# Kernel tuning notes

Measured on AMD Instinct MI355X. Metric: run time of the kernel, lower is better.

Reference implementation:

```python
import jax, jax.numpy as jnp
import numpy as np

S = 3072      # total tokens across all images
DIM = 1280    # hidden_size
H = 16        # num_heads
HD = DIM // H # head_dim = 80
NSEG = 6      # number of images (cu_seqlens has NSEG+1 entries)


def _rotate_half(x):
    x1, x2 = jnp.split(x, 2, axis=-1)
    return jnp.concatenate([-x2, x1], axis=-1)


def setup_inputs() -> dict:
    key = jax.random.key(0)
    ks = jax.random.split(key, 12)
    hidden_states = jax.random.normal(ks[0], (S, DIM), jnp.float32)
    # realistic vision rotary embedding: half-dim inv_freq, repeated to head_dim
    inv_freq = 1.0 / (10000.0 ** (jnp.arange(0, HD // 2, dtype=jnp.float32) / (HD // 2)))
    freqs = jnp.arange(S, dtype=jnp.float32)[:, None] * inv_freq[None, :]  # [S, HD/2]
    emb = jnp.concatenate([freqs, freqs], axis=-1)  # [S, HD]
    cos = jnp.cos(emb)
    sin = jnp.sin(emb)
    sc = 0.02
    wq = jax.random.normal(ks[1], (DIM, DIM), jnp.float32) * sc
    bq = jax.random.normal(ks[2], (DIM,), jnp.float32) * sc
    wk = jax.random.normal(ks[3], (DIM, DIM), jnp.float32) * sc
    bk = jax.random.normal(ks[4], (DIM,), jnp.float32) * sc
    wv = jax.random.normal(ks[5], (DIM, DIM), jnp.float32) * sc
    bv = jax.random.normal(ks[6], (DIM,), jnp.float32) * sc
    wo = jax.random.normal(ks[7], (DIM, DIM), jnp.float32) * sc
    bo = jax.random.normal(ks[8], (DIM,), jnp.float32) * sc
    cu_seqlens = (jnp.arange(NSEG + 1, dtype=jnp.int32) * (S // NSEG))  # [0,512,...,3072]
    return dict(hidden_states=hidden_states, cos=cos, sin=sin,
                wq=wq, bq=bq, wk=wk, bk=bk, wv=wv, bv=bv, wo=wo, bo=bo,
                cu_seqlens=cu_seqlens)


def reference(hidden_states, cos, sin, wq, bq, wk, bk, wv, bv, wo, bo, cu_seqlens):
    seq_length = hidden_states.shape[0]
    scaling = HD ** (-0.5)
    # QKV projections (torch Linear: x @ W.T + b)
    q = (hidden_states @ wq.T + bq).reshape(seq_length, H, HD)
    k = (hidden_states @ wk.T + bk).reshape(seq_length, H, HD)
    v = (hidden_states @ wv.T + bv).reshape(seq_length, H, HD)
    # apply_rotary_pos_emb_vision: cos/sin [S, HD] broadcast over head axis
    c = cos[:, None, :]
    s = sin[:, None, :]
    q = q * c + _rotate_half(q) * s
    k = k * c + _rotate_half(k) * s
    # block-diagonal (per-image) attention via segment mask
    seg = jnp.searchsorted(cu_seqlens[1:], jnp.arange(seq_length), side='right')
    mask = seg[:, None] == seg[None, :]  # [S, S] bool
    scores = jnp.einsum('shd,thd->hst', q, k) * scaling  # [H, S, S]
    scores = jnp.where(mask[None, :, :], scores, jnp.finfo(scores.dtype).min)
    attn = jax.nn.softmax(scores, axis=-1)
    out = jnp.einsum('hst,thd->shd', attn, v).reshape(seq_length, DIM)
    return out @ wo.T + bo
```

## Files before the change

kernel.cpp:

```cpp
#include <hip/hip_runtime.h>
#include <hip/hip_bf16.h>
#include <hip/hip_fp16.h>
#include <cstdint>
#include <cstddef>

typedef _Float16 f16;
typedef f16 f16x4 __attribute__((ext_vector_type(4)));
typedef f16 f16x8 __attribute__((ext_vector_type(8)));
typedef float f32x4 __attribute__((ext_vector_type(4)));

#define S_LEN 3072
#define DIM 1280
#define NH 16
#define HD 80
#define SEG 512

#define MFMA16F(a, b, c) __builtin_amdgcn_mfma_f32_16x16x32_f16((a), (b), (c), 0, 0, 0)

__device__ __forceinline__ void gl2lds16(const void* g, void* l) {
    __builtin_amdgcn_global_load_lds(
        (const __attribute__((address_space(1))) unsigned int*)g,
        (__attribute__((address_space(3))) unsigned int*)l, 16, 0, 0);
}

__global__ __launch_bounds__(256) void cvt_kernel(
    const float* __restrict__ hs,
    const float* __restrict__ wq, const float* __restrict__ wk,
    const float* __restrict__ wv, const float* __restrict__ wo,
    f16* __restrict__ hs16,
    f16* __restrict__ wq16, f16* __restrict__ wk16,
    f16* __restrict__ wv16, f16* __restrict__ wo16)
{
    const int m = blockIdx.y;
    const float* src; f16* dst; int n4;
    if (m == 0)      { src = hs; dst = hs16; n4 = S_LEN * DIM / 4; }
    else if (m == 1) { src = wq; dst = wq16; n4 = DIM * DIM / 4; }
    else if (m == 2) { src = wk; dst = wk16; n4 = DIM * DIM / 4; }
    else if (m == 3) { src = wv; dst = wv16; n4 = DIM * DIM / 4; }
    else             { src = wo; dst = wo16; n4 = DIM * DIM / 4; }
    int idx = blockIdx.x * 256 + threadIdx.x;
    if (idx >= n4) return;
    f32x4 v = *(const f32x4*)(src + (size_t)idx * 4);
    f16x4 o;
#pragma unroll
    for (int e = 0; e < 4; ++e) o[e] = (f16)v[e];
    *(f16x4*)(dst + (size_t)idx * 4) = o;
}

__global__ __launch_bounds__(256) void gemm_f16_kernel(
    const f16* __restrict__ A,
    const f16* __restrict__ W0, const f16* __restrict__ W1, const f16* __restrict__ W2,
    const float* __restrict__ b0, const float* __restrict__ b1, const float* __restrict__ b2,
    f16* __restrict__ O0, f16* __restrict__ O1, f16* __restrict__ O2,
    float* __restrict__ OF, int mode_base)
{
    const int mode = mode_base + blockIdx.z;
    const f16* W = (mode == 1) ? W1 : (mode == 2) ? W2 : W0;
    const float* bias = (mode == 1) ? b1 : (mode == 2) ? b2 : b0;

    __shared__ __align__(16) f16 As[128 * 32];
    __shared__ __align__(16) f16 Bs[128 * 32];

    const int tid = threadIdx.x;
    const int lane = tid & 63;
    const int lane15 = tid & 15;
    const int quad = lane >> 4;
    const int w = tid >> 6;
    const int wm = (w >> 1) * 64;
    const int wn = (w & 1) * 64;
    const int m0 = blockIdx.x * 128;
    const int n0 = blockIdx.y * 128;

    const int srow = w * 32 + (lane >> 2);
    const int scol = (lane & 3) * 8;
    const f16* gA0 = A + (size_t)(m0 + srow) * DIM + scol;
    const f16* gA1 = A + (size_t)(m0 + srow + 16) * DIM + scol;
    const f16* gB0 = W + (size_t)(n0 + srow) * DIM + scol;
    const f16* gB1 = W + (size_t)(n0 + srow + 16) * DIM + scol;
    f16* lA0 = As + (w * 32) * 32;
    f16* lA1 = As + (w * 32 + 16) * 32;
    f16* lB0 = Bs + (w * 32) * 32;
    f16* lB1 = Bs + (w * 32 + 16) * 32;

    f32x4 acc[4][4];
#pragma unroll
    for (int i = 0; i < 4; ++i)
#pragma unroll
        for (int j = 0; j < 4; ++j)
            acc[i][j] = (f32x4){0.f, 0.f, 0.f, 0.f};

    for (int kt = 0; kt < DIM / 32; ++kt) {
        __syncthreads();
        gl2lds16(gA0 + kt * 32, lA0);
        gl2lds16(gA1 + kt * 32, lA1);
        gl2lds16(gB0 + kt * 32, lB0);
        gl2lds16(gB1 + kt * 32, lB1);
        __syncthreads();

        f16x8 fa[4], fb[4];
#pragma unroll
        for (int i = 0; i < 4; ++i)
            fa[i] = *(const f16x8*)(As + (wm + i * 16 + lane15) * 32 + quad * 8);
#pragma unroll
        for (int j = 0; j < 4; ++j)
            fb[j] = *(const f16x8*)(Bs + (wn + j * 16 + lane15) * 32 + quad * 8);
#pragma unroll
        for (int i = 0; i < 4; ++i)
#pragma unroll
            for (int j = 0; j < 4; ++j)
                acc[i][j] = MFMA16F(fa[i], fb[j], acc[i][j]);
    }

    float bvv[4];
#pragma unroll
    for (int j = 0; j < 4; ++j)
        bvv[j] = bias[n0 + wn + j * 16 + lane15];

    if (mode == 3) {
#pragma unroll
        for (int i = 0; i < 4; ++i)
#pragma unroll
            for (int j = 0; j < 4; ++j)
#pragma unroll
                for (int r = 0; r < 4; ++r) {
                    int row = m0 + wm + i * 16 + quad * 4 + r;
                    int col = n0 + wn + j * 16 + lane15;
                    OF[(size_t)row * DIM + col] = acc[i][j][r] + bvv[j];
                }
    } else {
        f16* O = (mode == 0) ? O0 : (mode == 1) ? O1 : O2;
#pragma unroll
        for (int i = 0; i < 4; ++i)
#pragma unroll
            for (int j = 0; j < 4; ++j)
#pragma unroll
                for (int r = 0; r < 4; ++r) {
                    int row = m0 + wm + i * 16 + quad * 4 + r;
                    int col = n0 + wn + j * 16 + lane15;
                    O[(size_t)row * DIM + col] = (f16)(acc[i][j][r] + bvv[j]);
                }
    }
}

__global__ __launch_bounds__(256) void vtrans_kernel(
    const f16* __restrict__ v, f16* __restrict__ vT)
{
    const int h = blockIdx.x;
    const int s0 = blockIdx.y * 128;
    __shared__ __align__(16) f16 Ls[128 * 128];
    const int tid = threadIdx.x;
#pragma unroll
    for (int c = tid; c < 1280; c += 256) {
        int r = c / 10;
        int ch = c - r * 10;
        int chs = ch ^ ((r >> 3) & 7);
        *(f16x8*)(Ls + r * 128 + chs * 8) =
            *(const f16x8*)(v + (size_t)(s0 + r) * DIM + h * HD + ch * 8);
    }
    __syncthreads();
#pragma unroll
    for (int c = tid; c < 1280; c += 256) {
        int d = c >> 4;
        int sc = c & 15;
        f16x8 ov;
#pragma unroll
        for (int e = 0; e < 8; ++e) {
            int s = sc * 8 + e;
            ov[e] = Ls[s * 128 + (((d >> 3) ^ (sc & 7)) * 8) + (d & 7)];
        }
        *(f16x8*)(vT + (size_t)(h * HD + d) * S_LEN + s0 + sc * 8) = ov;
    }
}

__global__ __launch_bounds__(256) void rope_kernel(
    f16* __restrict__ qb, f16* __restrict__ kb,
    const float* __restrict__ cosb, const float* __restrict__ sinb)
{
    int idx = blockIdx.x * 256 + threadIdx.x;
    int c = idx % 5;
    int t = idx / 5;
    int h = t & 15; t >>= 4;
    int s = t % S_LEN;
    int which = t / S_LEN;
    f16* buf = which ? kb : qb;
    float scale = which ? 1.0f : 0.11180339887498948f;
    int j = c * 8;
    f32x4 ca = *(const f32x4*)(cosb + s * HD + j);
    f32x4 cb = *(const f32x4*)(cosb + s * HD + j + 4);
    f32x4 sna = *(const f32x4*)(sinb + s * HD + j);
    f32x4 snb = *(const f32x4*)(sinb + s * HD + j + 4);
    size_t base = (size_t)s * DIM + h * HD + j;
    f16x8 x1 = *(f16x8*)(buf + base);
    f16x8 x2 = *(f16x8*)(buf + base + 40);
    f16x8 o1, o2;
#pragma unroll
    for (int e = 0; e < 8; ++e) {
        float ce = (e < 4) ? ca[e] : cb[e - 4];
        float se = (e < 4) ? sna[e] : snb[e - 4];
        float a = (float)x1[e], b = (float)x2[e];
        o1[e] = (f16)((a * ce - b * se) * scale);
        o2[e] = (f16)((b * ce + a * se) * scale);
    }
    *(f16x8*)(buf + base) = o1;
    *(f16x8*)(buf + base + 40) = o2;
}

__global__ __launch_bounds__(256) void attn_kernel(
    const f16* __restrict__ q, const f16* __restrict__ k,
    const f16* __restrict__ vT, f16* __restrict__ o)
{
    const int h = blockIdx.x;
    const int g = blockIdx.y;
    const int qc = blockIdx.z;
    const int tid = threadIdx.x;
    const int lane15 = tid & 15;
    const int quad = (tid & 63) >> 4;
    const int w = tid >> 6;
    const int qbase = g * SEG + qc * 128;

    __shared__ __align__(16) f16 Ks[128 * 88];
    __shared__ __align__(16) f16 Vt[80 * 136];
    __shared__ __align__(16) f16 Ps[4][16 * 136];

    f16x8 zf;
#pragma unroll
    for (int e = 0; e < 8; ++e) zf[e] = (f16)0.0f;

    f16x8 fq[2][3];
#pragma unroll
    for (int mt = 0; mt < 2; ++mt) {
        const int row = qbase + w * 32 + mt * 16 + lane15;
#pragma unroll
        for (int kc = 0; kc < 3; ++kc) {
            if (kc == 2 && quad >= 2) fq[mt][kc] = zf;
            else fq[mt][kc] = *(const f16x8*)(q + (size_t)row * DIM + h * HD + kc * 32 + quad * 8);
        }
    }

    float m_run[2][4], l_run[2][4];
    f32x4 Oa[2][5];
#pragma unroll
    for (int mt = 0; mt < 2; ++mt) {
#pragma unroll
        for (int r = 0; r < 4; ++r) { m_run[mt][r] = -1e30f; l_run[mt][r] = 0.f; }
#pragma unroll
        for (int nt = 0; nt < 5; ++nt) Oa[mt][nt] = (f32x4){0.f, 0.f, 0.f, 0.f};
    }

    for (int kt = 0; kt < 4; ++kt) {
        __syncthreads();
        const int kb = g * SEG + kt * 128;
#pragma unroll
        for (int c = tid; c < 1280; c += 256) {
            int r = c / 10;
            int c8 = (c - r * 10) * 8;
            *(f16x8*)(Ks + r * 88 + c8) =
                *(const f16x8*)(k + (size_t)(kb + r) * DIM + h * HD + c8);
        }
#pragma unroll
        for (int c = tid; c < 1280; c += 256) {
            int d = c >> 4;
            int sc = (c & 15) * 8;
            *(f16x8*)(Vt + d * 136 + sc) =
                *(const f16x8*)(vT + (size_t)(h * HD + d) * S_LEN + kb + sc);
        }
        __syncthreads();

        f32x4 sa[2][8];
#pragma unroll
        for (int mt = 0; mt < 2; ++mt)
#pragma unroll
            for (int nt = 0; nt < 8; ++nt) sa[mt][nt] = (f32x4){0.f, 0.f, 0.f, 0.f};
#pragma unroll
        for (int kc = 0; kc < 3; ++kc) {
#pragma unroll
            for (int nt = 0; nt < 8; ++nt) {
                f16x8 fk;
                if (kc == 2 && quad >= 2) fk = zf;
                else fk = *(const f16x8*)(Ks + (nt * 16 + lane15) * 88 + kc * 32 + quad * 8);
                sa[0][nt] = MFMA16F(fq[0][kc], fk, sa[0][nt]);
                sa[1][nt] = MFMA16F(fq[1][kc], fk, sa[1][nt]);
            }
        }

#pragma unroll
        for (int mt = 0; mt < 2; ++mt) {
            float mtv[4];
#pragma unroll
            for (int r = 0; r < 4; ++r) mtv[r] = -1e30f;
#pragma unroll
            for (int nt = 0; nt < 8; ++nt)
#pragma unroll
                for (int r = 0; r < 4; ++r) mtv[r] = fmaxf(mtv[r], sa[mt][nt][r]);
#pragma unroll
            for (int off = 1; off < 16; off <<= 1)
#pragma unroll
                for (int r = 0; r < 4; ++r)
                    mtv[r] = fmaxf(mtv[r], __shfl_xor(mtv[r], off, 64));

            float alpha[4], lt[4];
#pragma unroll
            for (int r = 0; r < 4; ++r) {
                float mn = fmaxf(m_run[mt][r], mtv[r]);
                alpha[r] = __expf(m_run[mt][r] - mn);
                m_run[mt][r] = mn;
                lt[r] = 0.f;
            }
#pragma unroll
            for (int nt = 0; nt < 8; ++nt)
#pragma unroll
                for (int r = 0; r < 4; ++r) {
                    float p = __expf(sa[mt][nt][r] - m_run[mt][r]);
                    sa[mt][nt][r] = p;
                    lt[r] += p;
                }
#pragma unroll
            for (int off = 1; off < 16; off <<= 1)
#pragma unroll
                for (int r = 0; r < 4; ++r)
                    lt[r] += __shfl_xor(lt[r], off, 64);
#pragma unroll
            for (int r = 0; r < 4; ++r)
                l_run[mt][r] = l_run[mt][r] * alpha[r] + lt[r];

#pragma unroll
            for (int nt = 0; nt < 8; ++nt)
#pragma unroll
                for (int r = 0; r < 4; ++r)
                    Ps[w][(quad * 4 + r) * 136 + nt * 16 + lane15] = (f16)sa[mt][nt][r];

#pragma unroll
            for (int nt = 0; nt < 5; ++nt)
#pragma unroll
                for (int r = 0; r < 4; ++r) Oa[mt][nt][r] *= alpha[r];
#pragma unroll
            for (int kc2 = 0; kc2 < 4; ++kc2) {
                f16x8 fp = *(const f16x8*)(Ps[w] + lane15 * 136 + kc2 * 32 + quad * 8);
#pragma unroll
                for (int nt = 0; nt < 5; ++nt) {
                    f16x8 fv = *(const f16x8*)(Vt + (nt * 16 + lane15) * 136 + kc2 * 32 + quad * 8);
                    Oa[mt][nt] = MFMA16F(fp, fv, Oa[mt][nt]);
                }
            }
        }
    }

#pragma unroll
    for (int mt = 0; mt < 2; ++mt)
#pragma unroll
        for (int r = 0; r < 4; ++r) {
            float inv = 1.0f / l_run[mt][r];
            int row = qbase + w * 32 + mt * 16 + quad * 4 + r;
#pragma unroll
            for (int nt = 0; nt < 5; ++nt)
                o[(size_t)row * DIM + h * HD + nt * 16 + lane15] = (f16)(Oa[mt][nt][r] * inv);
        }
}

extern "C" void kernel_launch(void* const* d_in, const int* in_sizes, int n_in,
                              void* d_out, int out_size, void* d_ws, size_t ws_size,
                              hipStream_t stream)
{
    const float* hs   = (const float*)d_in[0];
    const float* cosb = (const float*)d_in[1];
    const float* sinb = (const float*)d_in[2];
    const float* wq   = (const float*)d_in[3];
    const float* bq   = (const float*)d_in[4];
    const float* wk   = (const float*)d_in[5];
    const float* bk   = (const float*)d_in[6];
    const float* wv   = (const float*)d_in[7];
    const float* bv   = (const float*)d_in[8];
    const float* wo   = (const float*)d_in[9];
    const float* bo   = (const float*)d_in[10];

    const size_t SD = (size_t)S_LEN * DIM;
    const size_t WW = (size_t)DIM * DIM;
    f16* hs16 = (f16*)d_ws;
    f16* wq16 = hs16 + SD;
    f16* wk16 = wq16 + WW;
    f16* wv16 = wk16 + WW;
    f16* wo16 = wv16 + WW;
    f16* q16  = wo16 + WW;
    f16* k16  = q16 + SD;
    f16* v16  = k16 + SD;
    f16* ao16 = v16 + SD;
    f16* vT16 = ao16 + SD;
    float* outb = (float*)d_out;

    cvt_kernel<<<dim3(S_LEN * DIM / 4 / 256, 5), 256, 0, stream>>>(
        hs, wq, wk, wv, wo, hs16, wq16, wk16, wv16, wo16);
    gemm_f16_kernel<<<dim3(24, 10, 3), 256, 0, stream>>>(
        hs16, wq16, wk16, wv16, bq, bk, bv, q16, k16, v16, nullptr, 0);
    vtrans_kernel<<<dim3(NH, 24), 256, 0, stream>>>(v16, vT16);
    rope_kernel<<<1920, 256, 0, stream>>>(q16, k16, cosb, sinb);
    attn_kernel<<<dim3(NH, 6, 4), 256, 0, stream>>>(q16, k16, vT16, ao16);
    gemm_f16_kernel<<<dim3(24, 10, 1), 256, 0, stream>>>(
        ao16, wo16, nullptr, nullptr, bo, nullptr, nullptr,
        nullptr, nullptr, nullptr, outb, 3);
}
```

Measured before the change: 238.1 us.

## Transpose attention MFMA so P stays in registers, halve query tile per block

The attention kernel now computes S^T (K as the A operand, Q as B), so each lane holds one query row's scores. Row max and sum need only two cross-lane shuffles, and P is repacked to fp16 and moved to the PV MFMA operand layout with register shuffles instead of going through LDS. Each block now handles 64 queries instead of 128, which doubles the grid to 768 blocks. The Vt tile uses an XOR swizzle in place of padding. K/V tiles are now loaded twice as often across the grid, and the shuffle-based repacking adds ALU work.

After: 226.3 us. 1.05x faster.

```diff
diff --git a/kernel.cpp b/kernel.cpp
--- a/kernel.cpp
+++ b/kernel.cpp
@@ -5,6 +5,7 @@
 #include <cstddef>
 
 typedef _Float16 f16;
+typedef f16 f16x2 __attribute__((ext_vector_type(2)));
 typedef f16 f16x4 __attribute__((ext_vector_type(4)));
 typedef f16 f16x8 __attribute__((ext_vector_type(8)));
 typedef float f32x4 __attribute__((ext_vector_type(4)));
@@ -21,6 +22,13 @@
     __builtin_amdgcn_global_load_lds(
         (const __attribute__((address_space(1))) unsigned int*)g,
         (__attribute__((address_space(3))) unsigned int*)l, 16, 0, 0);
+}
+
+__device__ __forceinline__ unsigned int pack2(float a, float b) {
+    f16x2 t = {(f16)a, (f16)b};
+    union { f16x2 v; unsigned int u; } c;
+    c.v = t;
+    return c.u;
 }
 
 __global__ __launch_bounds__(256) void cvt_kernel(
@@ -216,36 +224,27 @@
     const int lane15 = tid & 15;
     const int quad = (tid & 63) >> 4;
     const int w = tid >> 6;
-    const int qbase = g * SEG + qc * 128;
+    const int qbase = g * SEG + qc * 64;
+    const int qrow = qbase + w * 16 + lane15;
 
     __shared__ __align__(16) f16 Ks[128 * 88];
-    __shared__ __align__(16) f16 Vt[80 * 136];
-    __shared__ __align__(16) f16 Ps[4][16 * 136];
+    __shared__ __align__(16) f16 Vt[80 * 128];
 
     f16x8 zf;
 #pragma unroll
     for (int e = 0; e < 8; ++e) zf[e] = (f16)0.0f;
 
-    f16x8 fq[2][3];
-#pragma unroll
-    for (int mt = 0; mt < 2; ++mt) {
-        const int row = qbase + w * 32 + mt * 16 + lane15;
-#pragma unroll
-        for (int kc = 0; kc < 3; ++kc) {
-            if (kc == 2 && quad >= 2) fq[mt][kc] = zf;
-            else fq[mt][kc] = *(const f16x8*)(q + (size_t)row * DIM + h * HD + kc * 32 + quad * 8);
-        }
-    }
-
-    float m_run[2][4], l_run[2][4];
-    f32x4 Oa[2][5];
-#pragma unroll
-    for (int mt = 0; mt < 2; ++mt) {
-#pragma unroll
-        for (int r = 0; r < 4; ++r) { m_run[mt][r] = -1e30f; l_run[mt][r] = 0.f; }
-#pragma unroll
-        for (int nt = 0; nt < 5; ++nt) Oa[mt][nt] = (f32x4){0.f, 0.f, 0.f, 0.f};
-    }
+    f16x8 fq[3];
+#pragma unroll
+    for (int kc = 0; kc < 3; ++kc) {
+        if (kc == 2 && quad >= 2) fq[kc] = zf;
+        else fq[kc] = *(const f16x8*)(q + (size_t)qrow * DIM + h * HD + kc * 32 + quad * 8);
+    }
+
+    float m_run = -1e30f, l_run = 0.f;
+    f32x4 Oa[5];
+#pragma unroll
+    for (int dt = 0; dt < 5; ++dt) Oa[dt] = (f32x4){0.f, 0.f, 0.f, 0.f};
 
     for (int kt = 0; kt < 4; ++kt) {
         __syncthreads();
@@ -260,17 +259,15 @@
 #pragma unroll
         for (int c = tid; c < 1280; c += 256) {
             int d = c >> 4;
-            int sc = (c & 15) * 8;
-            *(f16x8*)(Vt + d * 136 + sc) =
-                *(const f16x8*)(vT + (size_t)(h * HD + d) * S_LEN + kb + sc);
+            int sc = c & 15;
+            *(f16x8*)(Vt + d * 128 + (sc ^ (d & 7)) * 8) =
+                *(const f16x8*)(vT + (size_t)(h * HD + d) * S_LEN + kb + sc * 8);
         }
         __syncthreads();
 
-        f32x4 sa[2][8];
-#pragma unroll
-        for (int mt = 0; mt < 2; ++mt)
-#pragma unroll
-            for (int nt = 0; nt < 8; ++nt) sa[mt][nt] = (f32x4){0.f, 0.f, 0.f, 0.f};
+        f32x4 sa[8];
+#pragma unroll
+        for (int nt = 0; nt < 8; ++nt) sa[nt] = (f32x4){0.f, 0.f, 0.f, 0.f};
 #pragma unroll
         for (int kc = 0; kc < 3; ++kc) {
 #pragma unroll
@@ -278,83 +275,78 @@
                 f16x8 fk;
                 if (kc == 2 && quad >= 2) fk = zf;
                 else fk = *(const f16x8*)(Ks + (nt * 16 + lane15) * 88 + kc * 32 + quad * 8);
-                sa[0][nt] = MFMA16F(fq[0][kc], fk, sa[0][nt]);
-                sa[1][nt] = MFMA16F(fq[1][kc], fk, sa[1][nt]);
+                sa[nt] = MFMA16F(fk, fq[kc], sa[nt]);
             }
         }
 
-#pragma unroll
-        for (int mt = 0; mt < 2; ++mt) {
-            float mtv[4];
-#pragma unroll
-            for (int r = 0; r < 4; ++r) mtv[r] = -1e30f;
-#pragma unroll
-            for (int nt = 0; nt < 8; ++nt)
-#pragma unroll
-                for (int r = 0; r < 4; ++r) mtv[r] = fmaxf(mtv[r], sa[mt][nt][r]);
-#pragma unroll
-            for (int off = 1; off < 16; off <<= 1)
-#pragma unroll
-                for (int r = 0; r < 4; ++r)
-                    mtv[r] = fmaxf(mtv[r], __shfl_xor(mtv[r], off, 64));
-
-            float alpha[4], lt[4];
-#pragma unroll
-            for (int r = 0; r < 4; ++r) {
-                float mn = fmaxf(m_run[mt][r], mtv[r]);
-                alpha[r] = __expf(m_run[mt][r] - mn);
-                m_run[mt][r] = mn;
-                lt[r] = 0.f;
+        float mt = -1e30f;
+#pragma unroll
+        for (int nt = 0; nt < 8; ++nt)
+#pragma unroll
+            for (int r = 0; r < 4; ++r) mt = fmaxf(mt, sa[nt][r]);
+        mt = fmaxf(mt, __shfl_xor(mt, 16, 64));
+        mt = fmaxf(mt, __shfl_xor(mt, 32, 64));
+
+        float mn = fmaxf(m_run, mt);
+        float alpha = __expf(m_run - mn);
+        m_run = mn;
+        float lt = 0.f;
+        unsigned int pp[8][2];
+#pragma unroll
+        for (int nt = 0; nt < 8; ++nt) {
+            float p0 = __expf(sa[nt][0] - mn);
+            float p1 = __expf(sa[nt][1] - mn);
+            float p2 = __expf(sa[nt][2] - mn);
+            float p3 = __expf(sa[nt][3] - mn);
+            lt += (p0 + p1) + (p2 + p3);
+            pp[nt][0] = pack2(p0, p1);
+            pp[nt][1] = pack2(p2, p3);
+        }
+        lt += __shfl_xor(lt, 16, 64);
+        lt += __shfl_xor(lt, 32, 64);
+        l_run = l_run * alpha + lt;
+
+#pragma unroll
+        for (int dt = 0; dt < 5; ++dt)
+#pragma unroll
+            for (int r = 0; r < 4; ++r) Oa[dt][r] *= alpha;
+
+        const int srcA = ((quad & 1) * 2) * 16 + lane15;
+        const int srcB = srcA + 16;
+        const bool hi = quad >= 2;
+#pragma unroll
+        for (int kc2 = 0; kc2 < 4; ++kc2) {
+            unsigned int e0 = __shfl((int)pp[2 * kc2][0], srcA, 64);
+            unsigned int e1 = __shfl((int)pp[2 * kc2][1], srcA, 64);
+            unsigned int e2 = __shfl((int)pp[2 * kc2][0], srcB, 64);
+            unsigned int e3 = __shfl((int)pp[2 * kc2][1], srcB, 64);
+            unsigned int o0 = __shfl((int)pp[2 * kc2 + 1][0], srcA, 64);
+            unsigned int o1 = __shfl((int)pp[2 * kc2 + 1][1], srcA, 64);
+            unsigned int o2 = __shfl((int)pp[2 * kc2 + 1][0], srcB, 64);
+            unsigned int o3 = __shfl((int)pp[2 * kc2 + 1][1], srcB, 64);
+            union { unsigned int u[4]; f16x8 v; } fp;
+            fp.u[0] = hi ? o0 : e0;
+            fp.u[1] = hi ? o1 : e1;
+            fp.u[2] = hi ? o2 : e2;
+            fp.u[3] = hi ? o3 : e3;
+#pragma unroll
+            for (int dt = 0; dt < 5; ++dt) {
+                int drow = dt * 16 + lane15;
+                int slot = (kc2 * 4 + quad) ^ (drow & 7);
+                f16x8 fv = *(const f16x8*)(Vt + drow * 128 + slot * 8);
+                Oa[dt] = MFMA16F(fv, fp.v, Oa[dt]);
             }
-#pragma unroll
-            for (int nt = 0; nt < 8; ++nt)
-#pragma unroll
-                for (int r = 0; r < 4; ++r) {
-                    float p = __expf(sa[mt][nt][r] - m_run[mt][r]);
-                    sa[mt][nt][r] = p;
-                    lt[r] += p;
-                }
-#pragma unroll
-            for (int off = 1; off < 16; off <<= 1)
-#pragma unroll
-                for (int r = 0; r < 4; ++r)
-                    lt[r] += __shfl_xor(lt[r], off, 64);
-#pragma unroll
-            for (int r = 0; r < 4; ++r)
-                l_run[mt][r] = l_run[mt][r] * alpha[r] + lt[r];
-
-#pragma unroll
-            for (int nt = 0; nt < 8; ++nt)
-#pragma unroll
-                for (int r = 0; r < 4; ++r)
-                    Ps[w][(quad * 4 + r) * 136 + nt * 16 + lane15] = (f16)sa[mt][nt][r];
-
-#pragma unroll
-            for (int nt = 0; nt < 5; ++nt)
-#pragma unroll
-                for (int r = 0; r < 4; ++r) Oa[mt][nt][r] *= alpha[r];
-#pragma unroll
-            for (int kc2 = 0; kc2 < 4; ++kc2) {
-                f16x8 fp = *(const f16x8*)(Ps[w] + lane15 * 136 + kc2 * 32 + quad * 8);
-#pragma unroll
-                for (int nt = 0; nt < 5; ++nt) {
-                    f16x8 fv = *(const f16x8*)(Vt + (nt * 16 + lane15) * 136 + kc2 * 32 + quad * 8);
-                    Oa[mt][nt] = MFMA16F(fp, fv, Oa[mt][nt]);
-                }
-            }
-        }
-    }
-
-#pragma unroll
-    for (int mt = 0; mt < 2; ++mt)
-#pragma unroll
-        for (int r = 0; r < 4; ++r) {
-            float inv = 1.0f / l_run[mt][r];
-            int row = qbase + w * 32 + mt * 16 + quad * 4 + r;
-#pragma unroll
-            for (int nt = 0; nt < 5; ++nt)
-                o[(size_t)row * DIM + h * HD + nt * 16 + lane15] = (f16)(Oa[mt][nt][r] * inv);
-        }
+        }
+    }
+
+    float inv = 1.0f / l_run;
+#pragma unroll
+    for (int dt = 0; dt < 5; ++dt) {
+        f16x4 ov;
+#pragma unroll
+        for (int r = 0; r < 4; ++r) ov[r] = (f16)(Oa[dt][r] * inv);
+        *(f16x4*)(o + (size_t)qrow * DIM + h * HD + dt * 16 + quad * 4) = ov;
+    }
 }
 
 extern "C" void kernel_launch(void* const* d_in, const int* in_sizes, int n_in,
@@ -393,7 +385,7 @@
         hs16, wq16, wk16, wv16, bq, bk, bv, q16, k16, v16, nullptr, 0);
     vtrans_kernel<<<dim3(NH, 24), 256, 0, stream>>>(v16, vT16);
     rope_kernel<<<1920, 256, 0, stream>>>(q16, k16, cosb, sinb);
-    attn_kernel<<<dim3(NH, 6, 4), 256, 0, stream>>>(q16, k16, vT16, ao16);
+    attn_kernel<<<dim3(NH, 6, 8), 256, 0, stream>>>(q16, k16, vT16, ao16);
     gemm_f16_kernel<<<dim3(24, 10, 1), 256, 0, stream>>>(
         ao16, wo16, nullptr, nullptr, bo, nullptr, nullptr,
         nullptr, nullptr, nullptr, outb, 3);
```
